# Kernel optimization log

Hardware: AMD Instinct MI355X
Metric: run time of the kernel (lower is better)

The kernel has to match this reference:

```python
import jax, jax.numpy as jnp
import numpy as np

D_IN = 1024
D_OUT = 1024
N_HEADS = 16
D_HEAD = D_OUT // N_HEADS


def setup_inputs() -> dict:
    key = jax.random.key(0)
    ks = jax.random.split(key, 6)
    s = 0.02
    return {
        "x": jax.random.normal(ks[0], (4, 2048, D_IN), dtype=jnp.float32),
        "wq": jax.random.normal(ks[1], (D_IN, D_OUT), dtype=jnp.float32) * s,
        "wk": jax.random.normal(ks[2], (D_IN, D_OUT), dtype=jnp.float32) * s,
        "wv": jax.random.normal(ks[3], (D_IN, D_OUT), dtype=jnp.float32) * s,
        "wo": jax.random.normal(ks[4], (D_OUT, D_OUT), dtype=jnp.float32) * s,
        "bo": jax.random.normal(ks[5], (D_OUT,), dtype=jnp.float32) * s,
    }


def reference(x, wq, wk, wv, wo, bo):
    B, T, _ = x.shape
    # QKV projections (no bias), split into heads: (B, H, T, Dh)
    def split_heads(t):
        return t.reshape(B, T, N_HEADS, D_HEAD).transpose(0, 2, 1, 3)
    q = split_heads(x @ wq)
    k = split_heads(x @ wk)
    v = split_heads(x @ wv)
    # attention scores (B, H, T, T), causal mask, scale by sqrt(d_head)
    scores = jnp.einsum("bhqd,bhkd->bhqk", q, k)
    causal = jnp.tril(jnp.ones((T, T), dtype=bool))
    scores = jnp.where(causal, scores, -jnp.inf)
    attn = jax.nn.softmax(scores / jnp.sqrt(jnp.float32(D_HEAD)), axis=-1)
    # dropout = 0.0 (eval) -> identity
    ctx = jnp.einsum("bhqk,bhkd->bhqd", attn, v)
    ctx = ctx.transpose(0, 2, 1, 3).reshape(B, T, D_OUT)
    return ctx @ wo + bo
```

## Files before the change

### kernel.cpp

```cpp
#include <hip/hip_runtime.h>
#include <stdint.h>


typedef unsigned short u16;
typedef __bf16 bf16x8 __attribute__((ext_vector_type(8)));
typedef short s16x4 __attribute__((ext_vector_type(4)));
typedef float f32x4 __attribute__((ext_vector_type(4)));

extern "C" __device__ float __ocml_native_exp2_f32(float);

__device__ __forceinline__ u16 f2bf(float f) {
  union { float f; unsigned u; } v; v.f = f;
  return (u16)((v.u + 0x7fffu + ((v.u >> 16) & 1u)) >> 16);
}

__device__ __forceinline__ void gl_lds16(const void* g, void* l) {
  __builtin_amdgcn_global_load_lds((__attribute__((address_space(1))) void*)g,
                                   (__attribute__((address_space(3))) void*)l,
                                   16, 0, 0);
}

__global__ __launch_bounds__(256) void conv_x_k(const float* __restrict__ x,
                                                u16* __restrict__ xb) {
  int i = (blockIdx.x * 256 + threadIdx.x) * 4;
  float4 v = *reinterpret_cast<const float4*>(x + i);
  ushort4 o;
  o.x = f2bf(v.x); o.y = f2bf(v.y); o.z = f2bf(v.z); o.w = f2bf(v.w);
  *reinterpret_cast<ushort4*>(xb + i) = o;
}

__global__ __launch_bounds__(256) void conv_w_k(const float* __restrict__ w0,
                                                const float* __restrict__ w1,
                                                const float* __restrict__ w2,
                                                const float* __restrict__ w3,
                                                u16* __restrict__ dst) {
  const float* src = blockIdx.z == 0 ? w0 : blockIdx.z == 1 ? w1
                   : blockIdx.z == 2 ? w2 : w3;
  u16* d = dst + (size_t)blockIdx.z * 1024 * 1024;
  __shared__ float tile[32][33];
  int n0 = blockIdx.x * 32, k0 = blockIdx.y * 32;
  int tx = threadIdx.x & 31, ty = threadIdx.x >> 5;
  #pragma unroll
  for (int r = 0; r < 32; r += 8)
    tile[ty + r][tx] = src[(k0 + ty + r) * 1024 + n0 + tx];
  __syncthreads();
  #pragma unroll
  for (int r = 0; r < 32; r += 8)
    d[(n0 + ty + r) * 1024 + k0 + tx] = f2bf(tile[tx][ty + r]);
}

#define SWZ128(row, chunk) ((row) * 128 + ((((chunk) ^ ((row) & 7))) << 4))

__global__ __launch_bounds__(256) void gemm_qkv_k(const u16* __restrict__ A,
                                                  const u16* __restrict__ Wt,
                                                  u16* __restrict__ qw,
                                                  u16* __restrict__ kw,
                                                  u16* __restrict__ vtw) {
  __shared__ u16 SM[32768];
  const int tid = threadIdx.x;
  const int wave = tid >> 6, lane = tid & 63;
  const int quad = lane >> 4, l15 = lane & 15;
  const int m0 = blockIdx.x * 128;
  const int which = blockIdx.y >> 3;
  const int n0 = (blockIdx.y & 7) * 128;
  const u16* Bt = Wt + which * (1024 * 1024);
  const int waveM = (wave >> 1) * 64, waveN = (wave & 1) * 64;

  const f32x4 fz = {0.f, 0.f, 0.f, 0.f};
  f32x4 acc[4][4];
  #pragma unroll
  for (int i = 0; i < 4; i++)
    #pragma unroll
    for (int j = 0; j < 4; j++) acc[i][j] = fz;

  const int lrow8 = lane >> 3, lchunk = lane & 7;
  const int gsw = (lchunk ^ lrow8) * 8;
  const u16* Agp[4];
  const u16* Bgp[4];
  #pragma unroll
  for (int i = 0; i < 4; i++) {
    Agp[i] = A + (m0 + i * 32 + wave * 8 + lrow8) * 1024 + gsw;
    Bgp[i] = Bt + (n0 + i * 32 + wave * 8 + lrow8) * 1024 + gsw;
  }

  #pragma unroll
  for (int i = 0; i < 4; i++) {
    gl_lds16(Agp[i], (char*)SM + i * 4096 + wave * 1024);
    gl_lds16(Bgp[i], (char*)SM + 32768 + i * 4096 + wave * 1024);
  }

  #pragma unroll
  for (int s = 0; s < 16; s++) {
    const int o = (s & 1) * 16384;
    __syncthreads();
    if (s < 15) {
      const int nxt = 16384 - o;
      const int koff = (s + 1) * 64;
      #pragma unroll
      for (int i = 0; i < 4; i++) {
        gl_lds16(Agp[i] + koff, (char*)SM + nxt + i * 4096 + wave * 1024);
        gl_lds16(Bgp[i] + koff, (char*)SM + 32768 + nxt + i * 4096 + wave * 1024);
      }
    }
    #pragma unroll
    for (int kk = 0; kk < 2; kk++) {
      bf16x8 af[4], bf[4];
      #pragma unroll
      for (int mi = 0; mi < 4; mi++)
        af[mi] = *reinterpret_cast<const bf16x8*>(
            (char*)SM + o + SWZ128(waveM + mi * 16 + l15, kk * 4 + quad));
      #pragma unroll
      for (int ni = 0; ni < 4; ni++)
        bf[ni] = *reinterpret_cast<const bf16x8*>(
            (char*)SM + 32768 + o + SWZ128(waveN + ni * 16 + l15, kk * 4 + quad));
      #pragma unroll
      for (int mi = 0; mi < 4; mi++)
        #pragma unroll
        for (int ni = 0; ni < 4; ni++)
          acc[mi][ni] = __builtin_amdgcn_mfma_f32_16x16x32_bf16(af[mi], bf[ni], acc[mi][ni], 0, 0, 0);
    }
  }

  if (which != 2) {
    #pragma unroll
    for (int mi = 0; mi < 4; mi++) {
      #pragma unroll
      for (int r = 0; r < 4; r++) {
        int m = m0 + waveM + mi * 16 + quad * 4 + r;
        int b = m >> 11, t = m & 2047;
        #pragma unroll
        for (int ni = 0; ni < 4; ni++) {
          int n = n0 + waveN + ni * 16 + l15;
          int h = n >> 6, d = n & 63;
          float v = acc[mi][ni][r];
          if (which == 0) qw[((b * 16 + h) * 2048 + t) * 64 + d] = f2bf(v * 0.18033688f);
          else            kw[((b * 16 + h) * 2048 + t) * 64 + d] = f2bf(v);
        }
      }
    }
  } else {
    __syncthreads();
    #pragma unroll
    for (int mi = 0; mi < 4; mi++)
      #pragma unroll
      for (int r = 0; r < 4; r++) {
        int ml = waveM + mi * 16 + quad * 4 + r;
        #pragma unroll
        for (int ni = 0; ni < 4; ni++) {
          int nl = waveN + ni * 16 + l15;
          int byte = nl * 256 + (((ml >> 3) ^ (nl & 7)) << 4) + (ml & 7) * 2;
          *(u16*)((char*)SM + byte) = f2bf(acc[mi][ni][r]);
        }
      }
    __syncthreads();
    const int b = m0 >> 11, t0 = m0 & 2047;
    #pragma unroll
    for (int i = 0; i < 8; i++) {
      int cid = tid + 256 * i;
      int nl = cid >> 4, tc = cid & 15;
      int tb = tc >> 3, cp = tc & 7;
      int gl = ((2 * cp) & 3) * 4 + ((2 * cp) >> 2);
      int gh = ((2 * cp + 1) & 3) * 4 + ((2 * cp + 1) >> 2);
      int ml0 = tb * 64 + gl * 4, ml1 = tb * 64 + gh * 4;
      s16x4 lo = *reinterpret_cast<const s16x4*>(
          (char*)SM + nl * 256 + (((ml0 >> 3) ^ (nl & 7)) << 4) + (ml0 & 7) * 2);
      s16x4 hi = *reinterpret_cast<const s16x4*>(
          (char*)SM + nl * 256 + (((ml1 >> 3) ^ (nl & 7)) << 4) + (ml1 & 7) * 2);
      union { s16x4 hh[2]; bf16x8 w; } uu;
      uu.hh[0] = lo; uu.hh[1] = hi;
      int n = n0 + nl;
      int h = n >> 6, d = n & 63;
      *reinterpret_cast<bf16x8*>(vtw + (((b * 16 + h) * 64 + d) * 2048 + t0 + tc * 8)) = uu.w;
    }
  }
}

__global__ __launch_bounds__(256) void attn_k(const u16* __restrict__ Q,
                                              const u16* __restrict__ K,
                                              const u16* __restrict__ Vt,
                                              u16* __restrict__ ctx) {
  __shared__ u16 Qs[64 * 64];
  __shared__ u16 Ks[2][64 * 64];
  __shared__ u16 Vs[2][64 * 64];
  const int tid = threadIdx.x;
  const int wave = tid >> 6, lane = tid & 63;
  const int quad = lane >> 4, l15 = lane & 15;
  const int bh = blockIdx.x;
  const int qt = 31 - (int)blockIdx.y;
  const int b = bh >> 4, h = bh & 15;

  const u16* Qg = Q + (bh * 2048 + qt * 64) * 64;
  const u16* Kg = K + bh * (2048 * 64);
  const u16* Vg = Vt + bh * (64 * 2048);

  const int lrow = tid >> 3;
  const int lsw = ((tid & 7) ^ (lrow & 7)) * 8;

  gl_lds16(Qg + lrow * 64 + lsw, (char*)Qs + wave * 1024);
  gl_lds16(Qg + (32 + lrow) * 64 + lsw, (char*)Qs + wave * 1024 + 4096);
  {
    char* KsB = (char*)Ks[0] + wave * 1024;
    char* VsB = (char*)Vs[0] + wave * 1024;
    gl_lds16(Kg + lrow * 64 + lsw, KsB);
    gl_lds16(Kg + (32 + lrow) * 64 + lsw, KsB + 4096);
    gl_lds16(Vg + lrow * 2048 + lsw, VsB);
    gl_lds16(Vg + (32 + lrow) * 2048 + lsw, VsB + 4096);
  }

  const s16x4 ones4 = {(short)0x3F80, (short)0x3F80, (short)0x3F80, (short)0x3F80};
  const f32x4 fz = {0.f, 0.f, 0.f, 0.f};
  f32x4 accO[4];
  f32x4 accL = fz;
  #pragma unroll
  for (int dt = 0; dt < 4; dt++) accO[dt] = fz;
  bf16x8 qf[2];

  #define SWZB(row, chunk) ((row) * 128 + (((chunk) ^ ((row) & 7)) << 4))

  for (int j = 0; j <= qt; j++) {
    const int cur = j & 1;
    __syncthreads();
    if (j < qt) {
      char* KsB = (char*)Ks[cur ^ 1] + wave * 1024;
      char* VsB = (char*)Vs[cur ^ 1] + wave * 1024;
      const int jr = (j + 1) * 64;
      gl_lds16(Kg + (jr + lrow) * 64 + lsw, KsB);
      gl_lds16(Kg + (jr + 32 + lrow) * 64 + lsw, KsB + 4096);
      gl_lds16(Vg + lrow * 2048 + jr + lsw, VsB);
      gl_lds16(Vg + (32 + lrow) * 2048 + jr + lsw, VsB + 4096);
    }
    if (j == 0) {
      #pragma unroll
      for (int kk = 0; kk < 2; kk++)
        qf[kk] = *reinterpret_cast<const bf16x8*>(
            (char*)Qs + SWZB(wave * 16 + l15, kk * 4 + quad));
    }

    f32x4 s[4];
    #pragma unroll
    for (int nt = 0; nt < 4; nt++) s[nt] = fz;
    #pragma unroll
    for (int kk = 0; kk < 2; kk++)
      #pragma unroll
      for (int nt = 0; nt < 4; nt++) {
        bf16x8 kf = *reinterpret_cast<const bf16x8*>(
            (char*)Ks[cur] + SWZB(nt * 16 + l15, kk * 4 + quad));
        s[nt] = __builtin_amdgcn_mfma_f32_16x16x32_bf16(kf, qf[kk], s[nt], 0, 0, 0);
      }

    if (j == qt) {
      const int qrow = wave * 16 + l15;
      #pragma unroll
      for (int nt = 0; nt < 4; nt++)
        #pragma unroll
        for (int r = 0; r < 4; r++)
          if (nt * 16 + quad * 4 + r > qrow) s[nt][r] = -1e30f;
    }

    s16x4 pf[4];
    #pragma unroll
    for (int nt = 0; nt < 4; nt++) {
      float p0 = __ocml_native_exp2_f32(s[nt][0]);
      float p1 = __ocml_native_exp2_f32(s[nt][1]);
      float p2 = __ocml_native_exp2_f32(s[nt][2]);
      float p3 = __ocml_native_exp2_f32(s[nt][3]);
      union { s16x4 v; unsigned u[2]; } pk;
      pk.u[0] = __builtin_amdgcn_perm(__float_as_uint(p1), __float_as_uint(p0),
                                      0x07060302u);
      pk.u[1] = __builtin_amdgcn_perm(__float_as_uint(p3), __float_as_uint(p2),
                                      0x07060302u);
      pf[nt] = pk.v;
    }

    union { bf16x8 w; s16x4 hh[2]; } vv[2][4];
    #pragma unroll
    for (int r2 = 0; r2 < 2; r2++)
      #pragma unroll
      for (int dt = 0; dt < 4; dt++) {
        int row = dt * 16 + l15;
        vv[r2][dt].w = *reinterpret_cast<const bf16x8*>(
            (char*)Vs[cur] + row * 128 + (((quad * 2 + r2) ^ (row & 7)) << 4));
      }
    #pragma unroll
    for (int kc = 0; kc < 4; kc++) {
      accL = __builtin_amdgcn_mfma_f32_16x16x16bf16_1k(pf[kc], ones4, accL, 0, 0, 0);
      #pragma unroll
      for (int dt = 0; dt < 4; dt++)
        accO[dt] = __builtin_amdgcn_mfma_f32_16x16x16bf16_1k(
            pf[kc], vv[kc >> 1][dt].hh[kc & 1], accO[dt], 0, 0, 0);
    }
  }
  #undef SWZB

  float inv[4];
  #pragma unroll
  for (int r = 0; r < 4; r++) inv[r] = 1.0f / accL[r];
  const int trow = qt * 64 + wave * 16 + quad * 4;
  #pragma unroll
  for (int dt = 0; dt < 4; dt++)
    #pragma unroll
    for (int r = 0; r < 4; r++)
      ctx[(b * 2048 + trow + r) * 1024 + h * 64 + dt * 16 + l15] =
          f2bf(accO[dt][r] * inv[r]);
}

__global__ __launch_bounds__(256) void gemm_out_k(const u16* __restrict__ A,
                                                  const u16* __restrict__ Wt,
                                                  const float* __restrict__ bo,
                                                  float* __restrict__ out) {
  __shared__ u16 SM[32768];
  const int tid = threadIdx.x;
  const int wave = tid >> 6, lane = tid & 63;
  const int quad = lane >> 4, l15 = lane & 15;
  const int m0 = blockIdx.x * 128;
  const int n0 = blockIdx.y * 128;
  const int waveM = (wave >> 1) * 64, waveN = (wave & 1) * 64;

  const f32x4 fz = {0.f, 0.f, 0.f, 0.f};
  f32x4 acc[4][4];
  #pragma unroll
  for (int i = 0; i < 4; i++)
    #pragma unroll
    for (int j = 0; j < 4; j++) acc[i][j] = fz;

  const int lrow8 = lane >> 3, lchunk = lane & 7;
  const int gsw = (lchunk ^ lrow8) * 8;
  const u16* Agp[4];
  const u16* Bgp[4];
  #pragma unroll
  for (int i = 0; i < 4; i++) {
    Agp[i] = A + (m0 + i * 32 + wave * 8 + lrow8) * 1024 + gsw;
    Bgp[i] = Wt + (n0 + i * 32 + wave * 8 + lrow8) * 1024 + gsw;
  }

  #pragma unroll
  for (int i = 0; i < 4; i++) {
    gl_lds16(Agp[i], (char*)SM + i * 4096 + wave * 1024);
    gl_lds16(Bgp[i], (char*)SM + 32768 + i * 4096 + wave * 1024);
  }

  #pragma unroll
  for (int s = 0; s < 16; s++) {
    const int o = (s & 1) * 16384;
    __syncthreads();
    if (s < 15) {
      const int nxt = 16384 - o;
      const int koff = (s + 1) * 64;
      #pragma unroll
      for (int i = 0; i < 4; i++) {
        gl_lds16(Agp[i] + koff, (char*)SM + nxt + i * 4096 + wave * 1024);
        gl_lds16(Bgp[i] + koff, (char*)SM + 32768 + nxt + i * 4096 + wave * 1024);
      }
    }
    #pragma unroll
    for (int kk = 0; kk < 2; kk++) {
      bf16x8 af[4], bf[4];
      #pragma unroll
      for (int mi = 0; mi < 4; mi++)
        af[mi] = *reinterpret_cast<const bf16x8*>(
            (char*)SM + o + SWZ128(waveM + mi * 16 + l15, kk * 4 + quad));
      #pragma unroll
      for (int ni = 0; ni < 4; ni++)
        bf[ni] = *reinterpret_cast<const bf16x8*>(
            (char*)SM + 32768 + o + SWZ128(waveN + ni * 16 + l15, kk * 4 + quad));
      #pragma unroll
      for (int mi = 0; mi < 4; mi++)
        #pragma unroll
        for (int ni = 0; ni < 4; ni++)
          acc[mi][ni] = __builtin_amdgcn_mfma_f32_16x16x32_bf16(af[mi], bf[ni], acc[mi][ni], 0, 0, 0);
    }
  }
  float bias[4];
  #pragma unroll
  for (int ni = 0; ni < 4; ni++) bias[ni] = bo[n0 + waveN + ni * 16 + l15];
  #pragma unroll
  for (int mi = 0; mi < 4; mi++)
    #pragma unroll
    for (int r = 0; r < 4; r++) {
      int m = m0 + waveM + mi * 16 + quad * 4 + r;
      #pragma unroll
      for (int ni = 0; ni < 4; ni++) {
        int n = n0 + waveN + ni * 16 + l15;
        out[(size_t)m * 1024 + n] = acc[mi][ni][r] + bias[ni];
      }
    }
}

extern "C" void kernel_launch(void* const* d_in, const int* in_sizes, int n_in,
                              void* d_out, int out_size, void* d_ws, size_t ws_size,
                              hipStream_t stream) {
  const float* x  = (const float*)d_in[0];
  const float* wq = (const float*)d_in[1];
  const float* wk = (const float*)d_in[2];
  const float* wv = (const float*)d_in[3];
  const float* wo = (const float*)d_in[4];
  const float* bo = (const float*)d_in[5];
  float* out = (float*)d_out;
  char* ws = (char*)d_ws;

  u16* xb  = (u16*)(ws);
  u16* wt  = (u16*)(ws + 16777216);
  u16* qw  = (u16*)(ws + 25165824);
  u16* kw  = (u16*)(ws + 41943040);
  u16* vtw = (u16*)(ws + 58720256);

  conv_x_k<<<8192, 256, 0, stream>>>(x, xb);
  conv_w_k<<<dim3(32, 32, 4), 256, 0, stream>>>(wq, wk, wv, wo, wt);
  gemm_qkv_k<<<dim3(64, 24), 256, 0, stream>>>(xb, wt, qw, kw, vtw);
  attn_k<<<dim3(64, 32), 256, 0, stream>>>(qw, kw, vtw, xb );
  gemm_out_k<<<dim3(64, 8), 256, 0, stream>>>(xb, wt + 3 * 1024 * 1024, bo, out);
}
```

Baseline: 228.6 us.

## Enlarge QKV GEMM tile to 256x256 with 512-thread blocks

The QKV projection GEMM moves from 128x128 tiles with 4 waves to 256x256 tiles with 8 waves, each wave computing a 128x64 sub-tile. B fragments are loaded once per k-step and reused across two M groups, which raises arithmetic intensity per LDS and global byte. LDS use grows to 128KB double-buffered and accumulator registers double, which cuts occupancy. The grid shrinks to 384 blocks, which may leave CUs underused.

```diff
diff --git a/kernel.cpp b/kernel.cpp
--- a/kernel.cpp
+++ b/kernel.cpp
@@ -51,88 +51,92 @@
 
 #define SWZ128(row, chunk) ((row) * 128 + ((((chunk) ^ ((row) & 7))) << 4))
 
-__global__ __launch_bounds__(256) void gemm_qkv_k(const u16* __restrict__ A,
-                                                  const u16* __restrict__ Wt,
-                                                  u16* __restrict__ qw,
-                                                  u16* __restrict__ kw,
-                                                  u16* __restrict__ vtw) {
-  __shared__ u16 SM[32768];
+__global__ __launch_bounds__(512, 2) void gemm_qkv_k(const u16* __restrict__ A,
+                                                     const u16* __restrict__ Wt,
+                                                     u16* __restrict__ qw,
+                                                     u16* __restrict__ kw,
+                                                     u16* __restrict__ vtw) {
+  __shared__ u16 SM[65536];
   const int tid = threadIdx.x;
   const int wave = tid >> 6, lane = tid & 63;
   const int quad = lane >> 4, l15 = lane & 15;
-  const int m0 = blockIdx.x * 128;
-  const int which = blockIdx.y >> 3;
-  const int n0 = (blockIdx.y & 7) * 128;
+  const int m0 = blockIdx.x * 256;
+  const int which = blockIdx.y >> 2;
+  const int n0 = (blockIdx.y & 3) * 256;
   const u16* Bt = Wt + which * (1024 * 1024);
-  const int waveM = (wave >> 1) * 64, waveN = (wave & 1) * 64;
+  const int waveM = (wave >> 2) * 128, waveN = (wave & 3) * 64;
 
   const f32x4 fz = {0.f, 0.f, 0.f, 0.f};
-  f32x4 acc[4][4];
-  #pragma unroll
-  for (int i = 0; i < 4; i++)
+  f32x4 acc[8][4];
+  #pragma unroll
+  for (int i = 0; i < 8; i++)
     #pragma unroll
     for (int j = 0; j < 4; j++) acc[i][j] = fz;
 
   const int lrow8 = lane >> 3, lchunk = lane & 7;
   const int gsw = (lchunk ^ lrow8) * 8;
-  const u16* Agp[4];
-  const u16* Bgp[4];
-  #pragma unroll
-  for (int i = 0; i < 4; i++) {
-    Agp[i] = A + (m0 + i * 32 + wave * 8 + lrow8) * 1024 + gsw;
-    Bgp[i] = Bt + (n0 + i * 32 + wave * 8 + lrow8) * 1024 + gsw;
-  }
-
-  #pragma unroll
-  for (int i = 0; i < 4; i++) {
-    gl_lds16(Agp[i], (char*)SM + i * 4096 + wave * 1024);
-    gl_lds16(Bgp[i], (char*)SM + 32768 + i * 4096 + wave * 1024);
-  }
-
-  #pragma unroll
+  const u16* Ag = A + (m0 + wave * 8 + lrow8) * 1024 + gsw;
+  const u16* Bg = Bt + (n0 + wave * 8 + lrow8) * 1024 + gsw;
+
+  auto stage = [&](int o, int ktv) {
+    #pragma unroll
+    for (int half = 0; half < 2; half++)
+      #pragma unroll
+      for (int i = 0; i < 2; i++) {
+        gl_lds16(Ag + (half * 128 + i * 64) * 1024 + ktv * 64,
+                 (char*)SM + o + half * 16384 + i * 8192 + wave * 1024);
+        gl_lds16(Bg + (half * 128 + i * 64) * 1024 + ktv * 64,
+                 (char*)SM + o + 32768 + half * 16384 + i * 8192 + wave * 1024);
+      }
+  };
+
+  stage(0, 0);
+
   for (int s = 0; s < 16; s++) {
-    const int o = (s & 1) * 16384;
+    const int o = (s & 1) * 65536;
     __syncthreads();
-    if (s < 15) {
-      const int nxt = 16384 - o;
-      const int koff = (s + 1) * 64;
-      #pragma unroll
-      for (int i = 0; i < 4; i++) {
-        gl_lds16(Agp[i] + koff, (char*)SM + nxt + i * 4096 + wave * 1024);
-        gl_lds16(Bgp[i] + koff, (char*)SM + 32768 + nxt + i * 4096 + wave * 1024);
-      }
-    }
-    #pragma unroll
-    for (int kk = 0; kk < 2; kk++) {
-      bf16x8 af[4], bf[4];
+    if (s < 15) stage(65536 - o, s + 1);
+
+    bf16x8 bfr[4][2];
+    #pragma unroll
+    for (int nj = 0; nj < 4; nj++)
+      #pragma unroll
+      for (int kk = 0; kk < 2; kk++)
+        bfr[nj][kk] = *reinterpret_cast<const bf16x8*>(
+            (char*)SM + o + 32768 + SWZ128(waveN + nj * 16 + l15, kk * 4 + quad));
+
+    #pragma unroll
+    for (int g = 0; g < 2; g++) {
+      bf16x8 af[4][2];
       #pragma unroll
       for (int mi = 0; mi < 4; mi++)
-        af[mi] = *reinterpret_cast<const bf16x8*>(
-            (char*)SM + o + SWZ128(waveM + mi * 16 + l15, kk * 4 + quad));
-      #pragma unroll
-      for (int ni = 0; ni < 4; ni++)
-        bf[ni] = *reinterpret_cast<const bf16x8*>(
-            (char*)SM + 32768 + o + SWZ128(waveN + ni * 16 + l15, kk * 4 + quad));
-      #pragma unroll
-      for (int mi = 0; mi < 4; mi++)
-        #pragma unroll
-        for (int ni = 0; ni < 4; ni++)
-          acc[mi][ni] = __builtin_amdgcn_mfma_f32_16x16x32_bf16(af[mi], bf[ni], acc[mi][ni], 0, 0, 0);
+        #pragma unroll
+        for (int kk = 0; kk < 2; kk++)
+          af[mi][kk] = *reinterpret_cast<const bf16x8*>(
+              (char*)SM + o + SWZ128(waveM + g * 64 + mi * 16 + l15, kk * 4 + quad));
+      #pragma unroll
+      for (int kk = 0; kk < 2; kk++)
+        #pragma unroll
+        for (int mi = 0; mi < 4; mi++)
+          #pragma unroll
+          for (int nj = 0; nj < 4; nj++)
+            acc[g * 4 + mi][nj] = __builtin_amdgcn_mfma_f32_16x16x32_bf16(
+                af[mi][kk], bfr[nj][kk], acc[g * 4 + mi][nj], 0, 0, 0);
     }
   }
 
   if (which != 2) {
     #pragma unroll
-    for (int mi = 0; mi < 4; mi++) {
+    for (int mi = 0; mi < 8; mi++) {
       #pragma unroll
       for (int r = 0; r < 4; r++) {
         int m = m0 + waveM + mi * 16 + quad * 4 + r;
         int b = m >> 11, t = m & 2047;
         #pragma unroll
-        for (int ni = 0; ni < 4; ni++) {
-          int n = n0 + waveN + ni * 16 + l15;
+        for (int nj = 0; nj < 4; nj++) {
+          int n = n0 + waveN + nj * 16 + l15;
           int h = n >> 6, d = n & 63;
-          float v = acc[mi][ni][r];
+          float v = acc[mi][nj][r];
           if (which == 0) qw[((b * 16 + h) * 2048 + t) * 64 + d] = f2bf(v * 0.18033688f);
           else            kw[((b * 16 + h) * 2048 + t) * 64 + d] = f2bf(v);
         }
@@ -141,36 +145,37 @@
   } else {
     __syncthreads();
     #pragma unroll
-    for (int mi = 0; mi < 4; mi++)
+    for (int mi = 0; mi < 8; mi++)
       #pragma unroll
       for (int r = 0; r < 4; r++) {
         int ml = waveM + mi * 16 + quad * 4 + r;
         #pragma unroll
-        for (int ni = 0; ni < 4; ni++) {
-          int nl = waveN + ni * 16 + l15;
-          int byte = nl * 256 + (((ml >> 3) ^ (nl & 7)) << 4) + (ml & 7) * 2;
-          *(u16*)((char*)SM + byte) = f2bf(acc[mi][ni][r]);
+        for (int nj = 0; nj < 4; nj++) {
+          int nl = waveN + nj * 16 + l15;
+          int byte = nl * 512 + ((((ml >> 3) ^ (nl & 7))) << 4) + (ml & 7) * 2;
+          *(u16*)((char*)SM + byte) = f2bf(acc[mi][nj][r]);
         }
       }
     __syncthreads();
     const int b = m0 >> 11, t0 = m0 & 2047;
     #pragma unroll
-    for (int i = 0; i < 8; i++) {
-      int cid = tid + 256 * i;
-      int nl = cid >> 4, tc = cid & 15;
-      int tb = tc >> 3, cp = tc & 7;
+    for (int i = 0; i < 16; i++) {
+      int cid = tid + 512 * i;
+      int nl = cid >> 5, tc = cid & 31;
+      int jb = tc >> 3, cp = tc & 7;
       int gl = ((2 * cp) & 3) * 4 + ((2 * cp) >> 2);
       int gh = ((2 * cp + 1) & 3) * 4 + ((2 * cp + 1) >> 2);
-      int ml0 = tb * 64 + gl * 4, ml1 = tb * 64 + gh * 4;
+      int ml0 = jb * 64 + gl * 4, ml1 = jb * 64 + gh * 4;
       s16x4 lo = *reinterpret_cast<const s16x4*>(
-          (char*)SM + nl * 256 + (((ml0 >> 3) ^ (nl & 7)) << 4) + (ml0 & 7) * 2);
+          (char*)SM + nl * 512 + (((ml0 >> 3) ^ (nl & 7)) << 4) + (ml0 & 7) * 2);
       s16x4 hi = *reinterpret_cast<const s16x4*>(
-          (char*)SM + nl * 256 + (((ml1 >> 3) ^ (nl & 7)) << 4) + (ml1 & 7) * 2);
+          (char*)SM + nl * 512 + (((ml1 >> 3) ^ (nl & 7)) << 4) + (ml1 & 7) * 2);
       union { s16x4 hh[2]; bf16x8 w; } uu;
       uu.hh[0] = lo; uu.hh[1] = hi;
       int n = n0 + nl;
       int h = n >> 6, d = n & 63;
-      *reinterpret_cast<bf16x8*>(vtw + (((b * 16 + h) * 64 + d) * 2048 + t0 + tc * 8)) = uu.w;
+      *reinterpret_cast<bf16x8*>(
+          vtw + (((size_t)(b * 16 + h) * 64 + d) * 2048 + t0 + tc * 8)) = uu.w;
     }
   }
 }
@@ -406,7 +411,7 @@
 
   conv_x_k<<<8192, 256, 0, stream>>>(x, xb);
   conv_w_k<<<dim3(32, 32, 4), 256, 0, stream>>>(wq, wk, wv, wo, wt);
-  gemm_qkv_k<<<dim3(64, 24), 256, 0, stream>>>(xb, wt, qw, kw, vtw);
+  gemm_qkv_k<<<dim3(32, 12), 512, 0, stream>>>(xb, wt, qw, kw, vtw);
   attn_k<<<dim3(64, 32), 256, 0, stream>>>(qw, kw, vtw, xb );
   gemm_out_k<<<dim3(64, 8), 256, 0, stream>>>(xb, wt + 3 * 1024 * 1024, bo, out);
 }
```

After: 241.7 us. 1.06x slower.
